# Kernel optimization log

Hardware: AMD Instinct MI355X
Metric: run time of the kernel (lower is better)

Reference implementation:

```python
import jax, jax.numpy as jnp
import numpy as np

NEG_SLOPE = 0.2

def setup_inputs() -> dict:
    key = jax.random.key(0)
    k1, k2, k3, k4, k5 = jax.random.split(key, 5)
    N_src, N_dst, E, H, D = 50000, 50000, 1600000, 8, 16
    return {
        "h_src": jax.random.normal(k1, (N_src, H * D), dtype=jnp.float32),
        "h_dst": jax.random.normal(k2, (N_dst, H * D), dtype=jnp.float32),
        "attn_l": jax.random.normal(k3, (1, H, D), dtype=jnp.float32),
        "src": jax.random.randint(k4, (E,), 0, N_src, dtype=jnp.int32),
        "dst": jax.random.randint(k5, (E,), 0, N_dst, dtype=jnp.int32),
    }

def reference(h_src, h_dst, attn_l, src, dst):
    N_dst = h_dst.shape[0]
    H, D = attn_l.shape[1], attn_l.shape[2]
    hs = h_src.reshape(-1, H, D)                       # [N_src, H, D]
    el = jnp.sum(hs * attn_l, axis=-1)                 # [N_src, H] per-node attn logit
    e = jax.nn.leaky_relu(el[src], NEG_SLOPE)          # [E, H] per-edge score
    # edge softmax over incoming edges of each dst node (stable)
    seg_max = jax.ops.segment_max(e, dst, num_segments=N_dst)   # [N_dst, H]
    ex = jnp.exp(e - seg_max[dst])                     # [E, H]
    denom = jax.ops.segment_sum(ex, dst, num_segments=N_dst)    # [N_dst, H]
    a = ex / denom[dst]                                # [E, H]
    # gather-multiply-scatter: u_mul_e then sum by dst
    m = hs[src] * a[:, :, None]                        # [E, H, D]
    out = jax.ops.segment_sum(m, dst, num_segments=N_dst)       # [N_dst, H, D]
    return out.reshape(N_dst, H * D)
```

## Files before the change

### kernel.cpp

```cpp
#include <hip/hip_runtime.h>

#define Hh 8
#define HD 128
#define NEG_SLOPE 0.2f
#define EPB 4096
#define KCAP 2560


__device__ __forceinline__ unsigned bfr(float f) {
    unsigned u = __float_as_uint(f);
    return (u + 0x7fffu + ((u >> 16) & 1u)) >> 16;
}
__device__ __forceinline__ unsigned pk(float a, float b) { return bfr(a) | (bfr(b) << 16); }

__global__ void __launch_bounds__(1024)
k1(const int* __restrict__ src, const int* __restrict__ dst,
   unsigned* __restrict__ tmp, int* __restrict__ blen,
   int E, int nblk, int nbf,
   const float* __restrict__ hs, const float* __restrict__ attn,
   float* __restrict__ ew, uint4* __restrict__ hsb, int nh_src) {
    int t = threadIdx.x;
    if ((int)blockIdx.x < nblk) {
        __shared__ unsigned wbuf[EPB];
        __shared__ int lh[800], cur[800];
        int base = blockIdx.x * EPB;
        int cnt = E - base; if (cnt > EPB) cnt = EPB;
        if (t < 800) lh[t] = 0;
        __syncthreads();
        int i = t * 4;
        bool vec = (i + 3 < cnt);
        if (vec) {
            int4 d = *(const int4*)(dst + base + i);
            int4 s = *(const int4*)(src + base + i);
            uint4 w;
            w.x = ((unsigned)d.x << 16) | (unsigned)s.x;
            w.y = ((unsigned)d.y << 16) | (unsigned)s.y;
            w.z = ((unsigned)d.z << 16) | (unsigned)s.z;
            w.w = ((unsigned)d.w << 16) | (unsigned)s.w;
            ((uint4*)wbuf)[t] = w;
            atomicAdd(&lh[d.x >> 6], 1);
            atomicAdd(&lh[d.y >> 6], 1);
            atomicAdd(&lh[d.z >> 6], 1);
            atomicAdd(&lh[d.w >> 6], 1);
        } else {
            for (int e = i; e < cnt; ++e) {
                int d = dst[base + e];
                wbuf[e] = ((unsigned)d << 16) | (unsigned)src[base + e];
                atomicAdd(&lh[d >> 6], 1);
            }
        }
        __syncthreads();
        if (t < nbf) cur[t] = atomicAdd(&blen[t * 16], lh[t]);
        __syncthreads();
        if (vec) {
            uint4 w = ((uint4*)wbuf)[t];
            int p;
            p = atomicAdd(&cur[w.x >> 22], 1);
            if (p < KCAP) tmp[(size_t)(w.x >> 22) * KCAP + p] = w.x;
            p = atomicAdd(&cur[w.y >> 22], 1);
            if (p < KCAP) tmp[(size_t)(w.y >> 22) * KCAP + p] = w.y;
            p = atomicAdd(&cur[w.z >> 22], 1);
            if (p < KCAP) tmp[(size_t)(w.z >> 22) * KCAP + p] = w.z;
            p = atomicAdd(&cur[w.w >> 22], 1);
            if (p < KCAP) tmp[(size_t)(w.w >> 22) * KCAP + p] = w.w;
        } else {
            for (int e = i; e < cnt; ++e) {
                unsigned w = wbuf[e];
                int p = atomicAdd(&cur[w >> 22], 1);
                if (p < KCAP) tmp[(size_t)(w >> 22) * KCAP + p] = w;
            }
        }
    } else {
        int i = ((int)blockIdx.x - nblk) * 1024 + t;
        if (i >= nh_src) return;
        int n = i >> 3, h = i & 7;
        const float4* a = (const float4*)(hs + (size_t)n * HD + h * 16);
        const float4* w = (const float4*)(attn + h * 16);
        float4 x0 = a[0], x1 = a[1], x2 = a[2], x3 = a[3];
        float4 w0 = w[0], w1 = w[1], w2 = w[2], w3 = w[3];
        float sv = x0.x * w0.x + x0.y * w0.y + x0.z * w0.z + x0.w * w0.w
                 + x1.x * w1.x + x1.y * w1.y + x1.z * w1.z + x1.w * w1.w
                 + x2.x * w2.x + x2.y * w2.y + x2.z * w2.z + x2.w * w2.w
                 + x3.x * w3.x + x3.y * w3.y + x3.z * w3.z + x3.w * w3.w;
        sv = (sv >= 0.f) ? sv : NEG_SLOPE * sv;
        ew[i] = __expf(sv);
        uint4 p0 = { pk(x0.x, x0.y), pk(x0.z, x0.w), pk(x1.x, x1.y), pk(x1.z, x1.w) };
        uint4 p1 = { pk(x2.x, x2.y), pk(x2.z, x2.w), pk(x3.x, x3.y), pk(x3.z, x3.w) };
        hsb[(size_t)n * 16 + h * 2]     = p0;
        hsb[(size_t)n * 16 + h * 2 + 1] = p1;
    }
}

#define ACC8(X, W) \
    a0.x += __uint_as_float((X).x << 16) * (W); \
    a0.y += __uint_as_float((X).x & 0xffff0000u) * (W); \
    a0.z += __uint_as_float((X).y << 16) * (W); \
    a0.w += __uint_as_float((X).y & 0xffff0000u) * (W); \
    a1.x += __uint_as_float((X).z << 16) * (W); \
    a1.y += __uint_as_float((X).z & 0xffff0000u) * (W); \
    a1.z += __uint_as_float((X).w << 16) * (W); \
    a1.w += __uint_as_float((X).w & 0xffff0000u) * (W);

__global__ void __launch_bounds__(1024)
kA(const unsigned* __restrict__ tmp, const int* __restrict__ blen,
   const uint4* __restrict__ hsb, const float* __restrict__ ew,
   float* __restrict__ out, int ndst) {
    __shared__ unsigned stg[KCAP], srt[KCAP];
    __shared__ int lh[64], cur[64], exs[65];
    int b = blockIdx.x, t = threadIdx.x;
    int n = blen[b * 16]; if (n > KCAP) n = KCAP;
    const unsigned* tp = tmp + (size_t)b * KCAP;
    for (int j = t; j < n; j += 1024) stg[j] = tp[j];
    if (t < 64) lh[t] = 0;
    __syncthreads();
    for (int j = t; j < n; j += 1024)
        atomicAdd(&lh[(stg[j] >> 16) & 63], 1);
    __syncthreads();
    if (t == 0) {
        int a = 0;
        for (int k = 0; k < 64; ++k) { exs[k] = a; a += lh[k]; }
        exs[64] = a;
    }
    __syncthreads();
    if (t < 64) cur[t] = exs[t];
    __syncthreads();
    for (int j = t; j < n; j += 1024) {
        unsigned w = stg[j];
        int p = atomicAdd(&cur[(w >> 16) & 63], 1);
        srt[p] = w;
    }
    __syncthreads();
    int wave = t >> 6, lane = t & 63;
    int q = lane & 15, slot = lane >> 4, h = q >> 1;
    for (int ld = wave; ld < 64; ld += 16) {
        int d = b * 64 + ld;
        if (d >= ndst) break;
        int j0 = exs[ld] + slot, j1 = exs[ld + 1];
        float4 a0 = {0.f, 0.f, 0.f, 0.f}, a1 = {0.f, 0.f, 0.f, 0.f};
        float ws = 0.f;
        int j = j0;
        for (; j + 12 < j1; j += 16) {
            int s0 = srt[j] & 0xffff,      s1 = srt[j + 4] & 0xffff;
            int s2 = srt[j + 8] & 0xffff,  s3 = srt[j + 12] & 0xffff;
            float w0 = ew[s0 * Hh + h], w1 = ew[s1 * Hh + h];
            float w2 = ew[s2 * Hh + h], w3 = ew[s3 * Hh + h];
            uint4 x0 = hsb[(size_t)s0 * 16 + q];
            uint4 x1 = hsb[(size_t)s1 * 16 + q];
            uint4 x2 = hsb[(size_t)s2 * 16 + q];
            uint4 x3 = hsb[(size_t)s3 * 16 + q];
            ACC8(x0, w0)
            ACC8(x1, w1)
            ACC8(x2, w2)
            ACC8(x3, w3)
            ws += w0 + w1 + w2 + w3;
        }
        for (; j < j1; j += 4) {
            int s0 = srt[j] & 0xffff;
            float w0 = ew[s0 * Hh + h];
            uint4 x0 = hsb[(size_t)s0 * 16 + q];
            ACC8(x0, w0)
            ws += w0;
        }
#pragma unroll
        for (int off = 16; off <= 32; off <<= 1) {
            a0.x += __shfl_xor(a0.x, off, 64);
            a0.y += __shfl_xor(a0.y, off, 64);
            a0.z += __shfl_xor(a0.z, off, 64);
            a0.w += __shfl_xor(a0.w, off, 64);
            a1.x += __shfl_xor(a1.x, off, 64);
            a1.y += __shfl_xor(a1.y, off, 64);
            a1.z += __shfl_xor(a1.z, off, 64);
            a1.w += __shfl_xor(a1.w, off, 64);
            ws   += __shfl_xor(ws,   off, 64);
        }
        if (lane < 16) {
            float r = (ws > 0.f) ? 1.0f / ws : 0.f;
            a0.x *= r; a0.y *= r; a0.z *= r; a0.w *= r;
            a1.x *= r; a1.y *= r; a1.z *= r; a1.w *= r;
            float4* op = (float4*)(out + (size_t)d * HD + q * 8);
            op[0] = a0;
            op[1] = a1;
        }
    }
}

extern "C" void kernel_launch(void* const* d_in, const int* in_sizes, int n_in,
                              void* d_out, int out_size, void* d_ws, size_t ws_size,
                              hipStream_t stream) {
    const float* h_src  = (const float*)d_in[0];
    const float* attn_l = (const float*)d_in[2];
    const int*   src    = (const int*)d_in[3];
    const int*   dst    = (const int*)d_in[4];
    float* out = (float*)d_out;

    const int N_src = in_sizes[0] / HD;
    const int N_dst = in_sizes[1] / HD;
    const int E     = in_sizes[3];
    const int NH_src = N_src * Hh;

    const int NBLK  = (E + EPB - 1) / EPB;
    const int NBF   = (N_dst + 63) >> 6;
    const int NB_EW = (NH_src + 1023) / 1024;

    unsigned short* hsb = (unsigned short*)d_ws;
    float* ew = (float*)(hsb + (size_t)N_src * HD);
    unsigned* tmp = (unsigned*)(ew + NH_src);
    int* blen = (int*)(tmp + (size_t)NBF * KCAP);

    hipMemsetAsync(blen, 0, (size_t)NBF * 16 * sizeof(int), stream);
    k1<<<NBLK + NB_EW, 1024, 0, stream>>>(src, dst, tmp, blen, E, NBLK, NBF,
                                          h_src, attn_l, ew, (uint4*)hsb, NH_src);
    kA<<<NBF, 1024, 0, stream>>>(tmp, blen, (const uint4*)hsb, ew, out, N_dst);
}
```

Before: 194.9 us.

## Coarsen global bucketing to 256-dst buckets and split each across four blocks

```diff
diff --git a/kernel.cpp b/kernel.cpp
--- a/kernel.cpp
+++ b/kernel.cpp
@@ -4,6 +4,7 @@
 #define HD 128
 #define NEG_SLOPE 0.2f
 #define EPB 4096
+#define CAP 12288
 #define KCAP 2560
 
 
@@ -16,58 +17,48 @@
 __global__ void __launch_bounds__(1024)
 k1(const int* __restrict__ src, const int* __restrict__ dst,
    unsigned* __restrict__ tmp, int* __restrict__ blen,
-   int E, int nblk, int nbf,
+   int E, int nblk,
    const float* __restrict__ hs, const float* __restrict__ attn,
    float* __restrict__ ew, uint4* __restrict__ hsb, int nh_src) {
     int t = threadIdx.x;
     if ((int)blockIdx.x < nblk) {
-        __shared__ unsigned wbuf[EPB];
-        __shared__ int lh[800], cur[800];
+        __shared__ int lh[256], cur[256];
+        if (t < 256) lh[t] = 0;
+        __syncthreads();
         int base = blockIdx.x * EPB;
         int cnt = E - base; if (cnt > EPB) cnt = EPB;
-        if (t < 800) lh[t] = 0;
-        __syncthreads();
         int i = t * 4;
+        int4 d, s;
         bool vec = (i + 3 < cnt);
         if (vec) {
-            int4 d = *(const int4*)(dst + base + i);
-            int4 s = *(const int4*)(src + base + i);
-            uint4 w;
-            w.x = ((unsigned)d.x << 16) | (unsigned)s.x;
-            w.y = ((unsigned)d.y << 16) | (unsigned)s.y;
-            w.z = ((unsigned)d.z << 16) | (unsigned)s.z;
-            w.w = ((unsigned)d.w << 16) | (unsigned)s.w;
-            ((uint4*)wbuf)[t] = w;
-            atomicAdd(&lh[d.x >> 6], 1);
-            atomicAdd(&lh[d.y >> 6], 1);
-            atomicAdd(&lh[d.z >> 6], 1);
-            atomicAdd(&lh[d.w >> 6], 1);
+            d = *(const int4*)(dst + base + i);
+            s = *(const int4*)(src + base + i);
+            atomicAdd(&lh[d.x >> 8], 1);
+            atomicAdd(&lh[d.y >> 8], 1);
+            atomicAdd(&lh[d.z >> 8], 1);
+            atomicAdd(&lh[d.w >> 8], 1);
+        } else {
+            for (int e = i; e < cnt; ++e) atomicAdd(&lh[dst[base + e] >> 8], 1);
+        }
+        __syncthreads();
+        if (t < 256) cur[t] = atomicAdd(&blen[t * 16], lh[t]);
+        __syncthreads();
+        if (vec) {
+            int p;
+            p = atomicAdd(&cur[d.x >> 8], 1);
+            tmp[(size_t)(d.x >> 8) * CAP + p] = ((unsigned)(d.x & 255) << 16) | (unsigned)s.x;
+            p = atomicAdd(&cur[d.y >> 8], 1);
+            tmp[(size_t)(d.y >> 8) * CAP + p] = ((unsigned)(d.y & 255) << 16) | (unsigned)s.y;
+            p = atomicAdd(&cur[d.z >> 8], 1);
+            tmp[(size_t)(d.z >> 8) * CAP + p] = ((unsigned)(d.z & 255) << 16) | (unsigned)s.z;
+            p = atomicAdd(&cur[d.w >> 8], 1);
+            tmp[(size_t)(d.w >> 8) * CAP + p] = ((unsigned)(d.w & 255) << 16) | (unsigned)s.w;
         } else {
             for (int e = i; e < cnt; ++e) {
-                int d = dst[base + e];
-                wbuf[e] = ((unsigned)d << 16) | (unsigned)src[base + e];
-                atomicAdd(&lh[d >> 6], 1);
-            }
-        }
-        __syncthreads();
-        if (t < nbf) cur[t] = atomicAdd(&blen[t * 16], lh[t]);
-        __syncthreads();
-        if (vec) {
-            uint4 w = ((uint4*)wbuf)[t];
-            int p;
-            p = atomicAdd(&cur[w.x >> 22], 1);
-            if (p < KCAP) tmp[(size_t)(w.x >> 22) * KCAP + p] = w.x;
-            p = atomicAdd(&cur[w.y >> 22], 1);
-            if (p < KCAP) tmp[(size_t)(w.y >> 22) * KCAP + p] = w.y;
-            p = atomicAdd(&cur[w.z >> 22], 1);
-            if (p < KCAP) tmp[(size_t)(w.z >> 22) * KCAP + p] = w.z;
-            p = atomicAdd(&cur[w.w >> 22], 1);
-            if (p < KCAP) tmp[(size_t)(w.w >> 22) * KCAP + p] = w.w;
-        } else {
-            for (int e = i; e < cnt; ++e) {
-                unsigned w = wbuf[e];
-                int p = atomicAdd(&cur[w >> 22], 1);
-                if (p < KCAP) tmp[(size_t)(w >> 22) * KCAP + p] = w;
+                int dd = dst[base + e];
+                int p = atomicAdd(&cur[dd >> 8], 1);
+                tmp[(size_t)(dd >> 8) * CAP + p] =
+                    ((unsigned)(dd & 255) << 16) | (unsigned)src[base + e];
             }
         }
     } else {
@@ -102,19 +93,22 @@
     a1.w += __uint_as_float((X).w & 0xffff0000u) * (W);
 
 __global__ void __launch_bounds__(1024)
-kA(const unsigned* __restrict__ tmp, const int* __restrict__ blen,
-   const uint4* __restrict__ hsb, const float* __restrict__ ew,
-   float* __restrict__ out, int ndst) {
-    __shared__ unsigned stg[KCAP], srt[KCAP];
+kA4(const unsigned* __restrict__ tmp, const int* __restrict__ blen,
+    const uint4* __restrict__ hsb, const float* __restrict__ ew,
+    float* __restrict__ out, int ndst) {
+    __shared__ unsigned srt[KCAP];
     __shared__ int lh[64], cur[64], exs[65];
-    int b = blockIdx.x, t = threadIdx.x;
-    int n = blen[b * 16]; if (n > KCAP) n = KCAP;
-    const unsigned* tp = tmp + (size_t)b * KCAP;
-    for (int j = t; j < n; j += 1024) stg[j] = tp[j];
+    int b = blockIdx.x >> 2, sub = blockIdx.x & 3;
+    int t = threadIdx.x;
+    int n = blen[b * 16]; if (n > CAP) n = CAP;
+    const unsigned* tp = tmp + (size_t)b * CAP;
+    int lo = sub * 64;
     if (t < 64) lh[t] = 0;
     __syncthreads();
-    for (int j = t; j < n; j += 1024)
-        atomicAdd(&lh[(stg[j] >> 16) & 63], 1);
+    for (int j = t; j < n; j += 1024) {
+        int ld = (tp[j] >> 16) & 255;
+        if ((ld >> 6) == sub) atomicAdd(&lh[ld - lo], 1);
+    }
     __syncthreads();
     if (t == 0) {
         int a = 0;
@@ -125,17 +119,21 @@
     if (t < 64) cur[t] = exs[t];
     __syncthreads();
     for (int j = t; j < n; j += 1024) {
-        unsigned w = stg[j];
-        int p = atomicAdd(&cur[(w >> 16) & 63], 1);
-        srt[p] = w;
+        unsigned w = tp[j];
+        int ld = (w >> 16) & 255;
+        if ((ld >> 6) == sub) {
+            int p = atomicAdd(&cur[ld - lo], 1);
+            if (p < KCAP) srt[p] = w;
+        }
     }
     __syncthreads();
     int wave = t >> 6, lane = t & 63;
     int q = lane & 15, slot = lane >> 4, h = q >> 1;
     for (int ld = wave; ld < 64; ld += 16) {
-        int d = b * 64 + ld;
+        int d = b * 256 + lo + ld;
         if (d >= ndst) break;
         int j0 = exs[ld] + slot, j1 = exs[ld + 1];
+        if (j1 > KCAP) j1 = KCAP;
         float4 a0 = {0.f, 0.f, 0.f, 0.f}, a1 = {0.f, 0.f, 0.f, 0.f};
         float ws = 0.f;
         int j = j0;
@@ -199,16 +197,16 @@
     const int NH_src = N_src * Hh;
 
     const int NBLK  = (E + EPB - 1) / EPB;
-    const int NBF   = (N_dst + 63) >> 6;
+    const int NBKT  = (N_dst + 255) / 256;
     const int NB_EW = (NH_src + 1023) / 1024;
 
     unsigned short* hsb = (unsigned short*)d_ws;
     float* ew = (float*)(hsb + (size_t)N_src * HD);
     unsigned* tmp = (unsigned*)(ew + NH_src);
-    int* blen = (int*)(tmp + (size_t)NBF * KCAP);
-
-    hipMemsetAsync(blen, 0, (size_t)NBF * 16 * sizeof(int), stream);
-    k1<<<NBLK + NB_EW, 1024, 0, stream>>>(src, dst, tmp, blen, E, NBLK, NBF,
+    int* blen = (int*)(tmp + (size_t)NBKT * CAP);
+
+    hipMemsetAsync(blen, 0, (size_t)NBKT * 16 * sizeof(int), stream);
+    k1<<<NBLK + NB_EW, 1024, 0, stream>>>(src, dst, tmp, blen, E, NBLK,
                                           h_src, attn_l, ew, (uint4*)hsb, NH_src);
-    kA<<<NBF, 1024, 0, stream>>>(tmp, blen, (const uint4*)hsb, ew, out, N_dst);
-}
+    kA4<<<NBKT * 4, 1024, 0, stream>>>(tmp, blen, (const uint4*)hsb, ew, out, N_dst);
+}
```

Result: no change. 194.5 us (-0.2%).
